# Performance work log

Measured on AMD Instinct MI355X. Metric: run time of the kernel, lower is better.

## Reference

```python
import jax, jax.numpy as jnp
import numpy as np

N_CH, LONG, LAT = 8, 64, 64
N = N_CH * LONG * LAT          # 32768 flattened node count
OUT = 16 * 16                  # output_size ** 2
BATCH = 512


def _build_adjacency(n, long_, lat):
    # Faithful reconstruction of the (intended) COO pattern in GNNLayer.__init__.
    rows, cols, vals = [], [], []
    for k in range(n):
        for j in range(0, long_ * lat, 3):
            rows += [k + j, k + j, j]
            cols += [k + j, j, k + j]
            vals += [1.0, 1.0, 1.0]
        for i in range(lat + 1, (long_ - 1) * lat - 1, 3):
            offs = [i - 1, i + 1, i + lat, i - lat,
                    i + lat - 1, i + lat + 1, i - lat - 1, i - lat + 1]
            for o in offs:
                rows.append(i); cols.append(k + o); vals.append(1.0)
            for o in offs:
                rows.append(k + o); cols.append(i); vals.append(1.0)
    return (np.asarray(rows, np.int32), np.asarray(cols, np.int32),
            np.asarray(vals, np.float32))


def setup_inputs() -> dict:
    key = jax.random.key(0)
    k1, k2, k3 = jax.random.split(key, 3)
    rows, cols, vals = _build_adjacency(N_CH, LONG, LAT)
    x = jax.random.normal(k1, (BATCH, N_CH, LONG, LAT), jnp.float32)
    W = jax.random.normal(k2, (OUT, N), jnp.float32) / np.sqrt(N)  # lin1.weight
    b = jax.random.normal(k3, (OUT,), jnp.float32) * 0.01          # lin1.bias
    return {"x": x, "W": W, "b": b,
            "vals": jnp.asarray(vals),
            "rows": jnp.asarray(rows), "cols": jnp.asarray(cols)}


def reference(x, W, b, vals, rows, cols):
    B = x.shape[0]
    xf = x.reshape(B, -1)                    # [B, N]
    # SpMM with duplicate-index accumulation (matches torch COO coalescing):
    gathered = xf[:, cols] * vals            # [B, nnz]
    h1 = jax.ops.segment_sum(gathered.T, rows, num_segments=N).T  # [B, N]
    return h1 @ W.T + b                      # [B, 256]
```

## Files before the change

### kernel.cpp

```cpp
#include <hip/hip_runtime.h>
#include <hip/hip_bf16.h>

#define N_NODES 32768
#define OUT_F   256
#define BATCH   512
#define ROWS_CAP 4352
#define KS       17
#define KSLICE   256
#define GBM 64
#define GBN 64
#define FOLD_BLOCKS (KS * OUT_F)
#define CV_BLOCKS   ((BATCH * ROWS_CAP / 8) / 256)
#define OUT_BLOCKS  ((BATCH * OUT_F) / 256)
#define HALO 72
#define WIN  400


typedef __attribute__((ext_vector_type(8))) short short8;
typedef __attribute__((ext_vector_type(4))) float f32x4;

__device__ __forceinline__ float bf2f(ushort u) {
    return __uint_as_float(((unsigned)u) << 16);
}
__device__ __forceinline__ ushort f2bf(float f) {
    unsigned u = __float_as_uint(f);
    return (ushort)((u + 0x7fffu + ((u >> 16) & 1u)) >> 16);
}
__device__ __forceinline__ bool inJ(int x) { return x >= 0 && x <= 4095 && x % 3 == 0; }
__device__ __forceinline__ bool inI(int x) { return x >= 65 && x <= 4028 && x % 3 == 2; }

__global__ __launch_bounds__(256) void k_fused(const float* __restrict__ W,
                                               const float* __restrict__ xf,
                                               const float* __restrict__ bias,
                                               ushort* __restrict__ wbf2,
                                               ushort* __restrict__ xbf,
                                               float* __restrict__ out) {
    __shared__ float lw[WIN];
    int bid = blockIdx.x, t = threadIdx.x;
    if (bid < FOLD_BLOCKS) {
        int chunk = bid >> 8;
        int o     = bid & 255;
        int c0    = chunk * 256;
        int rbase = c0 - HALO;
        const float* wrow = W + (long)o * N_NODES;
        if (t < WIN / 4) {
            int r = rbase + t * 4;
            float4 v = (r >= 0) ? *(const float4*)(wrow + r)
                                : make_float4(0.f, 0.f, 0.f, 0.f);
            *(float4*)(lw + t * 4) = v;
        }
        __syncthreads();
        const int soff[30] = {-65,-64,-63,-62,-61,-60,-59,-58,-57,-56,
                               -1,  0,  1,  2,  3,  4,  5,  6,  7,  8,
                               63, 64, 65, 66, 67, 68, 69, 70, 71, 72};
        const float smul[30] = {1,2,3,3,3,3,3,3,2,1,
                                1,1,2,2,2,2,2,2,1,1,
                                1,2,3,3,3,3,3,3,2,1};
        int c = c0 + t;
        int ci = t + HALO;
        float accJ = 0.f, accI = 0.f;
        int m1 = 0;
        #pragma unroll
        for (int k = 0; k < 8; ++k) {
            int j = c - k;
            if (inJ(j)) { ++m1; accJ += lw[ci - k]; }
        }
        if (m1) accJ += (float)m1 * lw[ci];
        if (inJ(c)) {
            #pragma unroll
            for (int k = 0; k < 8; ++k) accJ += lw[ci + k];
        }
        #pragma unroll
        for (int q = 0; q < 30; ++q) {
            if (inI(c - soff[q])) accI += smul[q] * lw[ci - soff[q]];
        }
        if (inI(c)) {
            #pragma unroll
            for (int q = 0; q < 30; ++q) accI += smul[q] * lw[ci + soff[q]];
        }
        wbf2[(long)o * ROWS_CAP + c] = f2bf(accJ + accI);
        return;
    }
    if (bid < FOLD_BLOCKS + CV_BLOCKS) {
        int idx = (bid - FOLD_BLOCKS) * 256 + t;
        int b  = idx / (ROWS_CAP / 8);
        int kc = (idx % (ROWS_CAP / 8)) * 8;
        float4 x0 = *(const float4*)(xf + (long)b * N_NODES + kc);
        float4 x1 = *(const float4*)(xf + (long)b * N_NODES + kc + 4);
        short8 o;
        o[0] = (short)f2bf(x0.x); o[1] = (short)f2bf(x0.y);
        o[2] = (short)f2bf(x0.z); o[3] = (short)f2bf(x0.w);
        o[4] = (short)f2bf(x1.x); o[5] = (short)f2bf(x1.y);
        o[6] = (short)f2bf(x1.z); o[7] = (short)f2bf(x1.w);
        *(short8*)(xbf + (long)b * ROWS_CAP + kc) = o;
        return;
    }
    int idx = (bid - FOLD_BLOCKS - CV_BLOCKS) * 256 + t;
    out[idx] = bias[idx & (OUT_F - 1)];
}

__global__ __launch_bounds__(256) void k_gemm(const ushort* __restrict__ xbf,
                                              const ushort* __restrict__ wbf2,
                                              float* __restrict__ out) {
    __shared__ ushort Ash[GBM * 40];
    __shared__ ushort Bsh[GBN * 40];
    int t = threadIdx.x;
    int w = t >> 6, lane = t & 63;
    int lrow = lane & 15, lseg = lane >> 4;
    int gm0 = blockIdx.x * GBM, gn0 = blockIdx.y * GBN, k0 = blockIdx.z * KSLICE;
    int row = t >> 2, kc = (t & 3) * 8;
    f32x4 acc[4] = {};
    for (int ks = 0; ks < KSLICE; ks += 32) {
        int kb = k0 + ks;
        __syncthreads();
        {
            short8 v = *(const short8*)(xbf + (long)(gm0 + row) * ROWS_CAP + kb + kc);
            *(short8*)(Ash + row * 40 + kc) = v;
        }
        {
            short8 v = *(const short8*)(wbf2 + (long)(gn0 + row) * ROWS_CAP + kb + kc);
            *(short8*)(Bsh + row * 40 + kc) = v;
        }
        __syncthreads();
        short8 af = *(const short8*)(Ash + (w * 16 + lrow) * 40 + lseg * 8);
        #pragma unroll
        for (int f = 0; f < 4; ++f) {
            short8 bf = *(const short8*)(Bsh + (f * 16 + lrow) * 40 + lseg * 8);
            acc[f] = __builtin_amdgcn_mfma_f32_16x16x32_bf16(af, bf, acc[f], 0, 0, 0);
        }
    }
    #pragma unroll
    for (int f = 0; f < 4; ++f)
        #pragma unroll
        for (int i = 0; i < 4; ++i) {
            int rowg = gm0 + w * 16 + lseg * 4 + i;
            int colg = gn0 + f * 16 + lrow;
            atomicAdd(&out[(long)rowg * OUT_F + colg], acc[f][i]);
        }
}

extern "C" void kernel_launch(void* const* d_in, const int* in_sizes, int n_in,
                              void* d_out, int out_size, void* d_ws, size_t ws_size,
                              hipStream_t stream) {
    const float* xf   = (const float*)d_in[0];
    const float* W    = (const float*)d_in[1];
    const float* bias = (const float*)d_in[2];

    char* base = (char*)d_ws;
    ushort* wbf2 = (ushort*)base;
    ushort* xbf  = wbf2 + (size_t)OUT_F * ROWS_CAP;

    k_fused<<<FOLD_BLOCKS + CV_BLOCKS + OUT_BLOCKS, 256, 0, stream>>>(
        W, xf, bias, wbf2, xbf, (float*)d_out);

    k_gemm<<<dim3(BATCH / GBM, OUT_F / GBN, KS), 256, 0, stream>>>(xbf, wbf2, (float*)d_out);
}
```

Baseline: 31.27 us.

## Fuse x bf16 conversion into GEMM loads and double-buffer LDS tiles

Drops the separate pass that converted x to bf16 into a workspace buffer. The GEMM now reads fp32 x directly and converts it in registers while staging into shared memory. The shared tiles are also double-buffered so that global loads for the next k-step overlap the MFMA work on the current one, with one barrier per step. This saves a global write and reread of the bf16 x copy, at the cost of more shared memory and register use per block. Since each x tile is read by four N-blocks, the conversion work is repeated across them.

```diff
diff --git a/kernel.cpp b/kernel.cpp
--- a/kernel.cpp
+++ b/kernel.cpp
@@ -7,10 +7,10 @@
 #define ROWS_CAP 4352
 #define KS       17
 #define KSLICE   256
+#define NSTEP    (KSLICE / 32)
 #define GBM 64
 #define GBN 64
 #define FOLD_BLOCKS (KS * OUT_F)
-#define CV_BLOCKS   ((BATCH * ROWS_CAP / 8) / 256)
 #define OUT_BLOCKS  ((BATCH * OUT_F) / 256)
 #define HALO 72
 #define WIN  400
@@ -30,10 +30,8 @@
 __device__ __forceinline__ bool inI(int x) { return x >= 65 && x <= 4028 && x % 3 == 2; }
 
 __global__ __launch_bounds__(256) void k_fused(const float* __restrict__ W,
-                                               const float* __restrict__ xf,
                                                const float* __restrict__ bias,
                                                ushort* __restrict__ wbf2,
-                                               ushort* __restrict__ xbf,
                                                float* __restrict__ out) {
     __shared__ float lw[WIN];
     int bid = blockIdx.x, t = threadIdx.x;
@@ -81,53 +79,62 @@
         wbf2[(long)o * ROWS_CAP + c] = f2bf(accJ + accI);
         return;
     }
-    if (bid < FOLD_BLOCKS + CV_BLOCKS) {
-        int idx = (bid - FOLD_BLOCKS) * 256 + t;
-        int b  = idx / (ROWS_CAP / 8);
-        int kc = (idx % (ROWS_CAP / 8)) * 8;
-        float4 x0 = *(const float4*)(xf + (long)b * N_NODES + kc);
-        float4 x1 = *(const float4*)(xf + (long)b * N_NODES + kc + 4);
-        short8 o;
-        o[0] = (short)f2bf(x0.x); o[1] = (short)f2bf(x0.y);
-        o[2] = (short)f2bf(x0.z); o[3] = (short)f2bf(x0.w);
-        o[4] = (short)f2bf(x1.x); o[5] = (short)f2bf(x1.y);
-        o[6] = (short)f2bf(x1.z); o[7] = (short)f2bf(x1.w);
-        *(short8*)(xbf + (long)b * ROWS_CAP + kc) = o;
-        return;
-    }
-    int idx = (bid - FOLD_BLOCKS - CV_BLOCKS) * 256 + t;
+    int idx = (bid - FOLD_BLOCKS) * 256 + t;
     out[idx] = bias[idx & (OUT_F - 1)];
 }
 
-__global__ __launch_bounds__(256) void k_gemm(const ushort* __restrict__ xbf,
+__global__ __launch_bounds__(256) void k_gemm(const float* __restrict__ xf,
                                               const ushort* __restrict__ wbf2,
                                               float* __restrict__ out) {
-    __shared__ ushort Ash[GBM * 40];
-    __shared__ ushort Bsh[GBN * 40];
+    __shared__ ushort Ash[2][GBM * 40];
+    __shared__ ushort Bsh[2][GBN * 40];
     int t = threadIdx.x;
     int w = t >> 6, lane = t & 63;
     int lrow = lane & 15, lseg = lane >> 4;
     int gm0 = blockIdx.x * GBM, gn0 = blockIdx.y * GBN, k0 = blockIdx.z * KSLICE;
     int row = t >> 2, kc = (t & 3) * 8;
+    const float*  pa = xf   + (long)(gm0 + row) * N_NODES  + k0 + kc;
+    const ushort* pb = wbf2 + (long)(gn0 + row) * ROWS_CAP + k0 + kc;
+
+    {
+        float4 x0 = *(const float4*)(pa);
+        float4 x1 = *(const float4*)(pa + 4);
+        short8 va;
+        va[0] = (short)f2bf(x0.x); va[1] = (short)f2bf(x0.y);
+        va[2] = (short)f2bf(x0.z); va[3] = (short)f2bf(x0.w);
+        va[4] = (short)f2bf(x1.x); va[5] = (short)f2bf(x1.y);
+        va[6] = (short)f2bf(x1.z); va[7] = (short)f2bf(x1.w);
+        *(short8*)(Ash[0] + row * 40 + kc) = va;
+        *(short8*)(Bsh[0] + row * 40 + kc) = *(const short8*)(pb);
+    }
+    __syncthreads();
+
     f32x4 acc[4] = {};
-    for (int ks = 0; ks < KSLICE; ks += 32) {
-        int kb = k0 + ks;
-        __syncthreads();
-        {
-            short8 v = *(const short8*)(xbf + (long)(gm0 + row) * ROWS_CAP + kb + kc);
-            *(short8*)(Ash + row * 40 + kc) = v;
+    for (int ks = 0; ks < NSTEP; ++ks) {
+        int cur = ks & 1;
+        bool more = (ks + 1) < NSTEP;
+        float4 x0, x1; short8 vb;
+        if (more) {
+            x0 = *(const float4*)(pa + (ks + 1) * 32);
+            x1 = *(const float4*)(pa + (ks + 1) * 32 + 4);
+            vb = *(const short8*)(pb + (ks + 1) * 32);
         }
-        {
-            short8 v = *(const short8*)(wbf2 + (long)(gn0 + row) * ROWS_CAP + kb + kc);
-            *(short8*)(Bsh + row * 40 + kc) = v;
+        short8 af = *(const short8*)(Ash[cur] + (w * 16 + lrow) * 40 + lseg * 8);
+        #pragma unroll
+        for (int f = 0; f < 4; ++f) {
+            short8 bf = *(const short8*)(Bsh[cur] + (f * 16 + lrow) * 40 + lseg * 8);
+            acc[f] = __builtin_amdgcn_mfma_f32_16x16x32_bf16(af, bf, acc[f], 0, 0, 0);
+        }
+        if (more) {
+            short8 va;
+            va[0] = (short)f2bf(x0.x); va[1] = (short)f2bf(x0.y);
+            va[2] = (short)f2bf(x0.z); va[3] = (short)f2bf(x0.w);
+            va[4] = (short)f2bf(x1.x); va[5] = (short)f2bf(x1.y);
+            va[6] = (short)f2bf(x1.z); va[7] = (short)f2bf(x1.w);
+            *(short8*)(Ash[cur ^ 1] + row * 40 + kc) = va;
+            *(short8*)(Bsh[cur ^ 1] + row * 40 + kc) = vb;
         }
         __syncthreads();
-        short8 af = *(const short8*)(Ash + (w * 16 + lrow) * 40 + lseg * 8);
-        #pragma unroll
-        for (int f = 0; f < 4; ++f) {
-            short8 bf = *(const short8*)(Bsh + (f * 16 + lrow) * 40 + lseg * 8);
-            acc[f] = __builtin_amdgcn_mfma_f32_16x16x32_bf16(af, bf, acc[f], 0, 0, 0);
-        }
     }
     #pragma unroll
     for (int f = 0; f < 4; ++f)
@@ -146,12 +153,9 @@
     const float* W    = (const float*)d_in[1];
     const float* bias = (const float*)d_in[2];
 
-    char* base = (char*)d_ws;
-    ushort* wbf2 = (ushort*)base;
-    ushort* xbf  = wbf2 + (size_t)OUT_F * ROWS_CAP;
+    ushort* wbf2 = (ushort*)d_ws;
 
-    k_fused<<<FOLD_BLOCKS + CV_BLOCKS + OUT_BLOCKS, 256, 0, stream>>>(
-        W, xf, bias, wbf2, xbf, (float*)d_out);
+    k_fused<<<FOLD_BLOCKS + OUT_BLOCKS, 256, 0, stream>>>(W, bias, wbf2, (float*)d_out);
 
-    k_gemm<<<dim3(BATCH / GBM, OUT_F / GBN, KS), 256, 0, stream>>>(xbf, wbf2, (float*)d_out);
+    k_gemm<<<dim3(BATCH / GBM, OUT_F / GBN, KS), 256, 0, stream>>>(xf, wbf2, (float*)d_out);
 }
```

Measured after the change: 30.71 us. About the same (-1.8%).
